# Kernel optimization log

Hardware: AMD Instinct MI355X
Metric: run time of the kernel (lower is better)

Reference implementation:

```python
import jax, jax.numpy as jnp
import numpy as np

B, T, C, KQ = 4096, 128, 20, 100
SCALE = 1.0 / np.sqrt(128.0)  # 1/sqrt(input_length)


def setup_inputs() -> dict:
    key = jax.random.key(0)
    ks = jax.random.split(key, 4)
    x = jax.random.normal(ks[0], (B, T, C), dtype=jnp.float32)
    Wk = jax.random.normal(ks[1], (C, KQ), dtype=jnp.float32) * (1.0 / np.sqrt(C))
    Wq = jax.random.normal(ks[2], (C, KQ), dtype=jnp.float32) * (1.0 / np.sqrt(C))
    Wv = jax.random.normal(ks[3], (C, C), dtype=jnp.float32) * (1.0 / np.sqrt(C))
    bk = jnp.zeros((KQ,), dtype=jnp.float32)
    bq = jnp.zeros((KQ,), dtype=jnp.float32)
    bv = jnp.zeros((C,), dtype=jnp.float32)
    return {"x": x, "Wk": Wk, "bk": bk, "Wq": Wq, "bq": bq, "Wv": Wv, "bv": bv}


def reference(x, Wk, bk, Wq, bq, Wv, bv):
    # Dropout layers are identity at inference.
    k = jax.nn.elu(jnp.einsum('btc,ck->btk', x, Wk) + bk)   # [B,T,KQ]
    q = jax.nn.elu(jnp.einsum('btc,ck->btk', x, Wq) + bq)   # [B,T,KQ]
    v = jnp.tanh(jnp.einsum('btc,cd->btd', x, Wv) + bv)      # [B,T,C]
    # batch_dot(k, q^T): scores[b, i, j] = sum_d k[b,i,d] * q[b,j,d]
    w = jnp.einsum('bid,bjd->bij', k, q) * SCALE              # [B,T,T]
    # Keras Softmax(axis=1): normalize over the first seq axis (rows)
    w = jax.nn.softmax(w, axis=1)
    y = jnp.einsum('bij,bjd->bid', w, v) + x                  # [B,T,C]
    return y
```

## Files before the change

### kernel.cpp

```cpp
#include <hip/hip_runtime.h>
#include <hip/hip_bf16.h>

#define T 128
#define C 20
#define KQ 100
#define NT 512
#define SCALE 0.08838834764831845f
#define K2E   0.12751744f
#define LOG2E 1.4426950408889634f
#define TWOL2E 2.885390081777927f
#define LDS8 136

typedef float  f32x4  __attribute__((ext_vector_type(4)));
typedef short  bf16x8 __attribute__((ext_vector_type(8)));
typedef unsigned int uint32;

__device__ __forceinline__ float exp2i(float x) { return __builtin_amdgcn_exp2f(x); }
__device__ __forceinline__ float rcpi(float x)  { return __builtin_amdgcn_rcpf(x); }

__device__ __forceinline__ short f2bf(float f) {
    unsigned u = __builtin_bit_cast(unsigned, f);
    unsigned r = (u + 0x7FFFu + ((u >> 16) & 1u)) >> 16;
    return (short)r;
}
__device__ __forceinline__ uint32 pk2(float a, float b) {
    __hip_bfloat162 h = __float22bfloat162_rn(float2{a, b});
    uint32 r;
    __builtin_memcpy(&r, &h, 4);
    return r;
}
__device__ __forceinline__ int pkfp8x4(float a, float b, float c, float d) {
    int r = __builtin_amdgcn_cvt_pk_fp8_f32(a, b, 0, false);
    r = __builtin_amdgcn_cvt_pk_fp8_f32(c, d, r, true);
    return r;
}
__device__ __forceinline__ unsigned char fp8_1(float a) {
    return (unsigned char)(__builtin_amdgcn_cvt_pk_fp8_f32(a, 0.f, 0, false) & 0xff);
}

__global__ void prep(const float* __restrict__ Wk, const float* __restrict__ bk,
                     const float* __restrict__ Wq, const float* __restrict__ bq,
                     const float* __restrict__ Wv, const float* __restrict__ bv,
                     short* __restrict__ wkT, short* __restrict__ wqT,
                     short* __restrict__ wvT)
{
    const int t = blockIdx.x * blockDim.x + threadIdx.x;
    if (t < 112 * 32) {
        const int n = t >> 5, c = t & 31;
        float vk = 0.f, vq = 0.f;
        if (n < KQ) {
            if (c < C)       { vk = Wk[c * KQ + n]; vq = Wq[c * KQ + n]; }
            else if (c == C) { vk = bk[n];          vq = bq[n]; }
        }
        wkT[t] = f2bf(vk);
        wqT[t] = f2bf(vq);
        if (t < 32 * 32) {
            const int n2 = t >> 5, c2 = t & 31;
            float vv = 0.f;
            if (n2 < C) {
                if (c2 < C)       vv = Wv[c2 * C + n2] * TWOL2E;
                else if (c2 == C) vv = bv[n2] * TWOL2E;
            }
            wvT[t] = f2bf(vv);
        }
    }
}

__global__ __launch_bounds__(NT, 8) void sa_fused(
    const float* __restrict__ x,
    const short* __restrict__ wAll,
    float* __restrict__ y)
{
    __shared__ __align__(16) unsigned char kp8[T * LDS8];
    __shared__ __align__(16) unsigned char q8 [T * LDS8];
    __shared__ __align__(16) unsigned char vT8[32 * LDS8];

    const int tid  = threadIdx.x;
    const int lane = tid & 63;
    const int w    = __builtin_amdgcn_readfirstlane(tid >> 6);
    const int quad = lane >> 4;
    const int l16  = lane & 15;
    const int b    = blockIdx.x;
    const float* xb = x + (size_t)b * (T * C);

    const float* xr = xb + (w * 16 + l16) * C;
    float4 f0, f1;
    f0 = (float4){0.f, 0.f, 0.f, 0.f};
    f1 = (float4){0.f, 0.f, 0.f, 0.f};
    if (quad < 2) {
        f0 = *(const float4*)(xr + quad * 8);
        f1 = *(const float4*)(xr + quad * 8 + 4);
    } else if (quad == 2) {
        f0 = *(const float4*)(xr + 16);
    }

    if (tid < T) {
        const uint2 z = {0u, 0u};
        *(uint2*)&kp8[tid * LDS8 + 112] = z;
        *(uint2*)&kp8[tid * LDS8 + 120] = z;
        *(uint2*)&q8 [tid * LDS8 + 112] = z;
        *(uint2*)&q8 [tid * LDS8 + 120] = z;
    }

    bf16x8 xf;
    {
        uint32 p0 = 0, p1 = 0, p2 = 0, p3 = 0;
        if (quad < 2) {
            p0 = pk2(f0.x, f0.y); p1 = pk2(f0.z, f0.w);
            p2 = pk2(f1.x, f1.y); p3 = pk2(f1.z, f1.w);
        } else if (quad == 2) {
            p0 = pk2(f0.x, f0.y); p1 = pk2(f0.z, f0.w);
            p2 = pk2(1.f, 0.f);
        }
        uint4 u4; u4.x = p0; u4.y = p1; u4.z = p2; u4.w = p3;
        xf = __builtin_bit_cast(bf16x8, u4);
    }

    #pragma unroll
    for (int grp = 0; grp < 4; ++grp) {
        bf16x8 wfr[4];
        #pragma unroll
        for (int t = 0; t < 4; ++t)
            wfr[t] = *(const bf16x8*)(wAll + ((grp * 4 + t) * 16 + l16) * 32 + quad * 8);
        #pragma unroll
        for (int s = 0; s < 4; ++s) {
            const int tt = grp * 4 + s;
            const f32x4 cc = __builtin_amdgcn_mfma_f32_16x16x32_bf16(
                wfr[s], xf, (f32x4){0.f, 0.f, 0.f, 0.f}, 0, 0, 0);
            if (tt < 14) {
                float e[4];
                #pragma unroll
                for (int r = 0; r < 4; ++r) {
                    const float z = cc[r];
                    e[r] = __builtin_amdgcn_fmed3f(z, exp2i(z * LOG2E) - 1.f, 0.f);
                }
                unsigned char* dst = (tt < 7)
                    ? &kp8[(w * 16 + l16) * LDS8 + tt * 16 + quad * 4]
                    : &q8 [(w * 16 + l16) * LDS8 + (tt - 7) * 16 + quad * 4];
                *(int*)dst = pkfp8x4(e[0], e[1], e[2], e[3]);
            } else {
                #pragma unroll
                for (int r = 0; r < 4; ++r) {
                    const float e2 = exp2i(cc[r]);
                    vT8[((tt - 14) * 16 + quad * 4 + r) * LDS8 + w * 16 + l16]
                        = fp8_1(fmaf(-2.f, rcpi(e2 + 1.f), 1.f));
                }
            }
        }
    }
    __syncthreads();

    f32x4 acc[8];
    #pragma unroll
    for (int nt = 0; nt < 8; ++nt) acc[nt] = (f32x4){0.f, 0.f, 0.f, 0.f};
    __builtin_amdgcn_s_setprio(1);
    #pragma unroll
    for (int ks = 0; ks < 4; ++ks) {
        const long a = *(const long*)&q8[(w * 16 + l16) * LDS8 + ks * 32 + quad * 8];
        #pragma unroll
        for (int nt = 0; nt < 8; ++nt) {
            const long bk8 = *(const long*)&kp8[(nt * 16 + l16) * LDS8 + ks * 32 + quad * 8];
            acc[nt] = __builtin_amdgcn_mfma_f32_16x16x32_fp8_fp8(a, bk8, acc[nt], 0, 0, 0);
        }
    }
    __builtin_amdgcn_s_setprio(0);

    float ssum[4] = {0.f, 0.f, 0.f, 0.f};
    #pragma unroll
    for (int nt = 0; nt < 8; ++nt)
        #pragma unroll
        for (int r = 0; r < 4; ++r) {
            const float e = exp2i(acc[nt][r] * K2E);
            acc[nt][r] = e;
            ssum[r] += e;
        }
    #pragma unroll
    for (int r = 0; r < 4; ++r) {
        float s = ssum[r];
        s += __shfl_xor(s, 1); s += __shfl_xor(s, 2);
        s += __shfl_xor(s, 4); s += __shfl_xor(s, 8);
        ssum[r] = 64.f * rcpi(s);
    }
    __syncthreads();

    #pragma unroll
    for (int nt = 0; nt < 8; ++nt) {
        *(int*)&kp8[(nt * 16 + l16) * LDS8 + w * 16 + quad * 4]
            = pkfp8x4(acc[nt][0] * ssum[0], acc[nt][1] * ssum[1],
                      acc[nt][2] * ssum[2], acc[nt][3] * ssum[3]);
    }
    __syncthreads();

    f32x4 yacc[2];
    yacc[0] = (f32x4){0.f, 0.f, 0.f, 0.f};
    yacc[1] = (f32x4){0.f, 0.f, 0.f, 0.f};
    __builtin_amdgcn_s_setprio(1);
    #pragma unroll
    for (int ks = 0; ks < 4; ++ks) {
        const long a = *(const long*)&kp8[(w * 16 + l16) * LDS8 + ks * 32 + quad * 8];
        #pragma unroll
        for (int nt = 0; nt < 2; ++nt) {
            const long bv8 = *(const long*)&vT8[(nt * 16 + l16) * LDS8 + ks * 32 + quad * 8];
            yacc[nt] = __builtin_amdgcn_mfma_f32_16x16x32_fp8_fp8(a, bv8, yacc[nt], 0, 0, 0);
        }
    }
    __builtin_amdgcn_s_setprio(0);

    {
        float* yb = y + (size_t)b * (T * C);
        const float inv64 = 1.f / 64.f;
        #pragma unroll
        for (int r = 0; r < 4; ++r) {
            const int row  = w * 16 + quad * 4 + r;
            const int base = row * C;
            yb[base + l16] = yacc[0][r] * inv64 + xb[base + l16];
            if (l16 < 4)
                yb[base + 16 + l16] = yacc[1][r] * inv64 + xb[base + 16 + l16];
        }
    }
}

extern "C" void kernel_launch(void* const* d_in, const int* in_sizes, int n_in,
                              void* d_out, int out_size, void* d_ws, size_t ws_size,
                              hipStream_t stream) {
    const float* x  = (const float*)d_in[0];
    const float* Wk = (const float*)d_in[1];
    const float* bk = (const float*)d_in[2];
    const float* Wq = (const float*)d_in[3];
    const float* bq = (const float*)d_in[4];
    const float* Wv = (const float*)d_in[5];
    const float* bv = (const float*)d_in[6];
    float* y = (float*)d_out;

    char* ws = (char*)d_ws;
    short* wkT = (short*)ws;
    short* wqT = (short*)(ws + 7168);
    short* wvT = (short*)(ws + 14336);

    prep<<<14, 256, 0, stream>>>(Wk, bk, Wq, bq, Wv, bv, wkT, wqT, wvT);

    const int B = in_sizes[0] / (T * C);
    sa_fused<<<B, NT, 0, stream>>>(x, (const short*)ws, y);
}
```

Measured before the change: 160.4 us.

## Halve block to 4 waves, each handling two 16-row tiles

Reduces the fused attention block from 8 to 4 wavefronts, with each wave processing two 16-row query tiles. K-fragment LDS loads in the score and PV MFMA loops are shared across both tiles, so LDS traffic per MFMA is halved. The cost is higher register pressure, since score accumulators double to 16 f32x4, and fewer waves per block to hide latency. The launch-bounds occupancy hint is lowered to match.

Measured after the change: 143.2 us. 1.12x faster.

```diff
diff --git a/kernel.cpp b/kernel.cpp
--- a/kernel.cpp
+++ b/kernel.cpp
@@ -4,7 +4,7 @@
 #define T 128
 #define C 20
 #define KQ 100
-#define NT 512
+#define NT 256
 #define SCALE 0.08838834764831845f
 #define K2E   0.12751744f
 #define LOG2E 1.4426950408889634f
@@ -66,7 +66,7 @@
     }
 }
 
-__global__ __launch_bounds__(NT, 8) void sa_fused(
+__global__ __launch_bounds__(NT, 4) void sa_fused(
     const float* __restrict__ x,
     const short* __restrict__ wAll,
     float* __restrict__ y)
@@ -83,15 +83,18 @@
     const int b    = blockIdx.x;
     const float* xb = x + (size_t)b * (T * C);
 
-    const float* xr = xb + (w * 16 + l16) * C;
-    float4 f0, f1;
-    f0 = (float4){0.f, 0.f, 0.f, 0.f};
-    f1 = (float4){0.f, 0.f, 0.f, 0.f};
-    if (quad < 2) {
-        f0 = *(const float4*)(xr + quad * 8);
-        f1 = *(const float4*)(xr + quad * 8 + 4);
-    } else if (quad == 2) {
-        f0 = *(const float4*)(xr + 16);
+    float4 fA[2], fB[2];
+    #pragma unroll
+    for (int h = 0; h < 2; ++h) {
+        const float* xr = xb + ((w + 4 * h) * 16 + l16) * C;
+        fA[h] = (float4){0.f, 0.f, 0.f, 0.f};
+        fB[h] = (float4){0.f, 0.f, 0.f, 0.f};
+        if (quad < 2) {
+            fA[h] = *(const float4*)(xr + quad * 8);
+            fB[h] = *(const float4*)(xr + quad * 8 + 4);
+        } else if (quad == 2) {
+            fA[h] = *(const float4*)(xr + 16);
+        }
     }
 
     if (tid < T) {
@@ -102,18 +105,19 @@
         *(uint2*)&q8 [tid * LDS8 + 120] = z;
     }
 
-    bf16x8 xf;
-    {
+    bf16x8 xf[2];
+    #pragma unroll
+    for (int h = 0; h < 2; ++h) {
         uint32 p0 = 0, p1 = 0, p2 = 0, p3 = 0;
         if (quad < 2) {
-            p0 = pk2(f0.x, f0.y); p1 = pk2(f0.z, f0.w);
-            p2 = pk2(f1.x, f1.y); p3 = pk2(f1.z, f1.w);
+            p0 = pk2(fA[h].x, fA[h].y); p1 = pk2(fA[h].z, fA[h].w);
+            p2 = pk2(fB[h].x, fB[h].y); p3 = pk2(fB[h].z, fB[h].w);
         } else if (quad == 2) {
-            p0 = pk2(f0.x, f0.y); p1 = pk2(f0.z, f0.w);
+            p0 = pk2(fA[h].x, fA[h].y); p1 = pk2(fA[h].z, fA[h].w);
             p2 = pk2(1.f, 0.f);
         }
         uint4 u4; u4.x = p0; u4.y = p1; u4.z = p2; u4.w = p3;
-        xf = __builtin_bit_cast(bf16x8, u4);
+        xf[h] = __builtin_bit_cast(bf16x8, u4);
     }
 
     #pragma unroll
@@ -125,83 +129,104 @@
         #pragma unroll
         for (int s = 0; s < 4; ++s) {
             const int tt = grp * 4 + s;
-            const f32x4 cc = __builtin_amdgcn_mfma_f32_16x16x32_bf16(
-                wfr[s], xf, (f32x4){0.f, 0.f, 0.f, 0.f}, 0, 0, 0);
-            if (tt < 14) {
-                float e[4];
-                #pragma unroll
-                for (int r = 0; r < 4; ++r) {
-                    const float z = cc[r];
-                    e[r] = __builtin_amdgcn_fmed3f(z, exp2i(z * LOG2E) - 1.f, 0.f);
+            #pragma unroll
+            for (int h = 0; h < 2; ++h) {
+                const int row = (w + 4 * h) * 16 + l16;
+                const f32x4 cc = __builtin_amdgcn_mfma_f32_16x16x32_bf16(
+                    wfr[s], xf[h], (f32x4){0.f, 0.f, 0.f, 0.f}, 0, 0, 0);
+                if (tt < 14) {
+                    float e[4];
+                    #pragma unroll
+                    for (int r = 0; r < 4; ++r) {
+                        const float z = cc[r];
+                        e[r] = __builtin_amdgcn_fmed3f(z, exp2i(z * LOG2E) - 1.f, 0.f);
+                    }
+                    unsigned char* dst = (tt < 7)
+                        ? &kp8[row * LDS8 + tt * 16 + quad * 4]
+                        : &q8 [row * LDS8 + (tt - 7) * 16 + quad * 4];
+                    *(int*)dst = pkfp8x4(e[0], e[1], e[2], e[3]);
+                } else {
+                    #pragma unroll
+                    for (int r = 0; r < 4; ++r) {
+                        const float e2 = exp2i(cc[r]);
+                        vT8[((tt - 14) * 16 + quad * 4 + r) * LDS8 + row]
+                            = fp8_1(fmaf(-2.f, rcpi(e2 + 1.f), 1.f));
+                    }
                 }
-                unsigned char* dst = (tt < 7)
-                    ? &kp8[(w * 16 + l16) * LDS8 + tt * 16 + quad * 4]
-                    : &q8 [(w * 16 + l16) * LDS8 + (tt - 7) * 16 + quad * 4];
-                *(int*)dst = pkfp8x4(e[0], e[1], e[2], e[3]);
-            } else {
-                #pragma unroll
-                for (int r = 0; r < 4; ++r) {
-                    const float e2 = exp2i(cc[r]);
-                    vT8[((tt - 14) * 16 + quad * 4 + r) * LDS8 + w * 16 + l16]
-                        = fp8_1(fmaf(-2.f, rcpi(e2 + 1.f), 1.f));
-                }
             }
         }
     }
     __syncthreads();
 
-    f32x4 acc[8];
-    #pragma unroll
-    for (int nt = 0; nt < 8; ++nt) acc[nt] = (f32x4){0.f, 0.f, 0.f, 0.f};
+    f32x4 acc[2][8];
+    #pragma unroll
+    for (int h = 0; h < 2; ++h)
+        #pragma unroll
+        for (int nt = 0; nt < 8; ++nt) acc[h][nt] = (f32x4){0.f, 0.f, 0.f, 0.f};
     __builtin_amdgcn_s_setprio(1);
     #pragma unroll
     for (int ks = 0; ks < 4; ++ks) {
-        const long a = *(const long*)&q8[(w * 16 + l16) * LDS8 + ks * 32 + quad * 8];
+        const long a0 = *(const long*)&q8[( w      * 16 + l16) * LDS8 + ks * 32 + quad * 8];
+        const long a1 = *(const long*)&q8[((w + 4) * 16 + l16) * LDS8 + ks * 32 + quad * 8];
         #pragma unroll
         for (int nt = 0; nt < 8; ++nt) {
             const long bk8 = *(const long*)&kp8[(nt * 16 + l16) * LDS8 + ks * 32 + quad * 8];
-            acc[nt] = __builtin_amdgcn_mfma_f32_16x16x32_fp8_fp8(a, bk8, acc[nt], 0, 0, 0);
+            acc[0][nt] = __builtin_amdgcn_mfma_f32_16x16x32_fp8_fp8(a0, bk8, acc[0][nt], 0, 0, 0);
+            acc[1][nt] = __builtin_amdgcn_mfma_f32_16x16x32_fp8_fp8(a1, bk8, acc[1][nt], 0, 0, 0);
         }
     }
     __builtin_amdgcn_s_setprio(0);
 
-    float ssum[4] = {0.f, 0.f, 0.f, 0.f};
-    #pragma unroll
-    for (int nt = 0; nt < 8; ++nt)
+    float ssum[2][4];
+    #pragma unroll
+    for (int h = 0; h < 2; ++h) {
+        #pragma unroll
+        for (int r = 0; r < 4; ++r) ssum[h][r] = 0.f;
+        #pragma unroll
+        for (int nt = 0; nt < 8; ++nt)
+            #pragma unroll
+            for (int r = 0; r < 4; ++r) {
+                const float e = exp2i(acc[h][nt][r] * K2E);
+                acc[h][nt][r] = e;
+                ssum[h][r] += e;
+            }
         #pragma unroll
         for (int r = 0; r < 4; ++r) {
-            const float e = exp2i(acc[nt][r] * K2E);
-            acc[nt][r] = e;
-            ssum[r] += e;
-        }
-    #pragma unroll
-    for (int r = 0; r < 4; ++r) {
-        float s = ssum[r];
-        s += __shfl_xor(s, 1); s += __shfl_xor(s, 2);
-        s += __shfl_xor(s, 4); s += __shfl_xor(s, 8);
-        ssum[r] = 64.f * rcpi(s);
+            float s = ssum[h][r];
+            s += __shfl_xor(s, 1); s += __shfl_xor(s, 2);
+            s += __shfl_xor(s, 4); s += __shfl_xor(s, 8);
+            ssum[h][r] = 64.f * rcpi(s);
+        }
     }
     __syncthreads();
 
     #pragma unroll
     for (int nt = 0; nt < 8; ++nt) {
         *(int*)&kp8[(nt * 16 + l16) * LDS8 + w * 16 + quad * 4]
-            = pkfp8x4(acc[nt][0] * ssum[0], acc[nt][1] * ssum[1],
-                      acc[nt][2] * ssum[2], acc[nt][3] * ssum[3]);
+            = pkfp8x4(acc[0][nt][0] * ssum[0][0], acc[0][nt][1] * ssum[0][1],
+                      acc[0][nt][2] * ssum[0][2], acc[0][nt][3] * ssum[0][3]);
+        *(int*)&kp8[(nt * 16 + l16) * LDS8 + (w + 4) * 16 + quad * 4]
+            = pkfp8x4(acc[1][nt][0] * ssum[1][0], acc[1][nt][1] * ssum[1][1],
+                      acc[1][nt][2] * ssum[1][2], acc[1][nt][3] * ssum[1][3]);
     }
     __syncthreads();
 
-    f32x4 yacc[2];
-    yacc[0] = (f32x4){0.f, 0.f, 0.f, 0.f};
-    yacc[1] = (f32x4){0.f, 0.f, 0.f, 0.f};
+    f32x4 yacc[2][2];
+    #pragma unroll
+    for (int h = 0; h < 2; ++h) {
+        yacc[h][0] = (f32x4){0.f, 0.f, 0.f, 0.f};
+        yacc[h][1] = (f32x4){0.f, 0.f, 0.f, 0.f};
+    }
     __builtin_amdgcn_s_setprio(1);
     #pragma unroll
     for (int ks = 0; ks < 4; ++ks) {
-        const long a = *(const long*)&kp8[(w * 16 + l16) * LDS8 + ks * 32 + quad * 8];
+        const long a0 = *(const long*)&kp8[( w      * 16 + l16) * LDS8 + ks * 32 + quad * 8];
+        const long a1 = *(const long*)&kp8[((w + 4) * 16 + l16) * LDS8 + ks * 32 + quad * 8];
         #pragma unroll
         for (int nt = 0; nt < 2; ++nt) {
             const long bv8 = *(const long*)&vT8[(nt * 16 + l16) * LDS8 + ks * 32 + quad * 8];
-            yacc[nt] = __builtin_amdgcn_mfma_f32_16x16x32_fp8_fp8(a, bv8, yacc[nt], 0, 0, 0);
+            yacc[0][nt] = __builtin_amdgcn_mfma_f32_16x16x32_fp8_fp8(a0, bv8, yacc[0][nt], 0, 0, 0);
+            yacc[1][nt] = __builtin_amdgcn_mfma_f32_16x16x32_fp8_fp8(a1, bv8, yacc[1][nt], 0, 0, 0);
         }
     }
     __builtin_amdgcn_s_setprio(0);
@@ -210,13 +235,15 @@
         float* yb = y + (size_t)b * (T * C);
         const float inv64 = 1.f / 64.f;
         #pragma unroll
-        for (int r = 0; r < 4; ++r) {
-            const int row  = w * 16 + quad * 4 + r;
-            const int base = row * C;
-            yb[base + l16] = yacc[0][r] * inv64 + xb[base + l16];
-            if (l16 < 4)
-                yb[base + 16 + l16] = yacc[1][r] * inv64 + xb[base + 16 + l16];
-        }
+        for (int h = 0; h < 2; ++h)
+            #pragma unroll
+            for (int r = 0; r < 4; ++r) {
+                const int row  = (w + 4 * h) * 16 + quad * 4 + r;
+                const int base = row * C;
+                yb[base + l16] = yacc[h][0][r] * inv64 + xb[base + l16];
+                if (l16 < 4)
+                    yb[base + 16 + l16] = yacc[h][1][r] * inv64 + xb[base + 16 + l16];
+            }
     }
 }
 
```
